# Optimization experiments

Hardware: AMD Instinct MI355X
Metric: run time of the kernel (lower is better)

## Reference

```python
import jax, jax.numpy as jnp
import numpy as np

NUM_INSTANCES = 8
NUM_HEADS = 4
EPS = 1e-12  # F.normalize eps


def _l2norm(t):
    # F.normalize(t, dim=-1): t / max(||t||_2, eps) along last axis
    n = jnp.sqrt(jnp.sum(t * t, axis=-1, keepdims=True))
    return t / jnp.maximum(n, EPS)


def setup_inputs() -> dict:
    key = jax.random.key(0)
    ks = jax.random.split(key, 10)
    B, C, H, W = 8, 256, 32, 32
    I = NUM_INSTANCES
    s = 0.05
    return {
        "x": jax.random.normal(ks[0], (B, C, H, W), dtype=jnp.float32),
        "w_inst": jax.random.normal(ks[1], (I, C), dtype=jnp.float32) * s,
        "b_inst": jnp.zeros((I,), dtype=jnp.float32),
        "w_q": jax.random.normal(ks[2], (C, C), dtype=jnp.float32) * s,
        "b_q": jnp.zeros((C,), dtype=jnp.float32),
        "w_k": jax.random.normal(ks[3], (C, C), dtype=jnp.float32) * s,
        "b_k": jnp.zeros((C,), dtype=jnp.float32),
        "w_v": jax.random.normal(ks[4], (C, C), dtype=jnp.float32) * s,
        "b_v": jnp.zeros((C,), dtype=jnp.float32),
    }


def reference(x, w_inst, b_inst, w_q, b_q, w_k, b_k, w_v, b_v):
    B, C, H, W = x.shape
    HW = H * W
    hd = C // NUM_HEADS
    scale = 1.0 / jnp.sqrt(jnp.float32(hd))

    # instance_conv (1x1) + softmax over instance axis
    inst = jnp.einsum('ic,bchw->bihw', w_inst, x) + b_inst[None, :, None, None]
    inst = jax.nn.softmax(inst, axis=1)          # [B, I, H, W]
    masks = jnp.transpose(inst, (1, 0, 2, 3))    # [I, B, H, W] for scan

    def step(acc, mask):                          # mask: [B, H, W]
        feat = (x * mask[:, None]).reshape(B, C, HW)  # masked features
        q = (jnp.einsum('oc,bcn->bon', w_q, feat) + b_q[:, None]).reshape(B, NUM_HEADS, hd, HW)
        k = (jnp.einsum('oc,bcn->bon', w_k, feat) + b_k[:, None]).reshape(B, NUM_HEADS, hd, HW)
        v = (jnp.einsum('oc,bcn->bon', w_v, feat) + b_v[:, None]).reshape(B, NUM_HEADS, hd, HW)
        q = _l2norm(q)
        k = _l2norm(k)
        scores = jnp.einsum('bhci,bhcj->bhij', q, k) * scale  # [B,h,HW,HW]
        attn = jax.nn.softmax(scores, axis=-1)
        att = jnp.einsum('bhij,bhcj->bhci', attn, v).reshape(B, C, H, W)
        return acc + att * mask[:, None], None

    out, _ = jax.lax.scan(step, jnp.zeros_like(x), masks)
    return out
```

## Files before the change

### kernel.cpp

```cpp
#include <hip/hip_runtime.h>
#include <hip/hip_fp16.h>

#define NB 8
#define NC 256
#define NHW 1024
#define NI 8
#define NH 4
#define HD 64
#define EPS 1e-12f
#define QSC  64.0f
#define QSCI 0.015625f

typedef _Float16 f16;
typedef __attribute__((ext_vector_type(8))) _Float16 half8;
typedef __attribute__((ext_vector_type(4))) float floatx4;

union H8 { half8 h8; __half2 h2[4]; uint4 u4; f16 e[8]; };
union H4 { uint2 u2; __half2 h2[2]; f16 e[4]; };
union PK { __half2 h2; unsigned u; };

__device__ __forceinline__ void gll16(const void* g, void* l) {
    __builtin_amdgcn_global_load_lds(
        (const __attribute__((address_space(1))) unsigned int*)g,
        (__attribute__((address_space(3))) unsigned int*)l, 16, 0, 0);
}

__global__ __launch_bounds__(256) void k_mask_part(
    const float* __restrict__ x, const float* __restrict__ w_inst,
    float* __restrict__ part_m, f16* __restrict__ xt)
{
    __shared__ __align__(16) f16 xls[32][264];
    int nt = blockIdx.x, b = blockIdx.y, cc = blockIdx.z;
    int tid = threadIdx.x;
    int n = nt*256 + tid;
    const float* xp = x + ((size_t)(b*NC + cc*32))*NHW + n;
    const float* wp = w_inst + cc*32;
    float acc[NI] = {};
#pragma unroll
    for (int c = 0; c < 32; ++c) {
        float xv = xp[(size_t)c*NHW];
        xls[c][tid] = (f16)xv;
#pragma unroll
        for (int i = 0; i < NI; ++i) acc[i] = fmaf(wp[i*NC + c], xv, acc[i]);
    }
#pragma unroll
    for (int i = 0; i < NI; ++i)
        part_m[((size_t)(cc*NI + i)*NB + b)*NHW + n] = acc[i];
    __syncthreads();
#pragma unroll
    for (int it = 0; it < 4; ++it) {
        int r = (tid >> 2) + it*64;
        int c8 = (tid & 3)*8;
        H8 v;
#pragma unroll
        for (int i = 0; i < 8; ++i) v.e[i] = xls[c8 + i][r];
        *(uint4*)(xt + ((size_t)(b*NHW + nt*256 + r))*NC + cc*32 + c8) = v.u4;
    }
}

__global__ __launch_bounds__(256) void k_gemm_mfma(
    const f16* __restrict__ xt,
    const float* __restrict__ wq, const float* __restrict__ wk, const float* __restrict__ wv,
    f16* __restrict__ Gqt, f16* __restrict__ Gkt, f16* __restrict__ Gv)
{
    __shared__ __align__(16) char glds[30720];
    int tid = threadIdx.x;
    int nt = blockIdx.x, ot = blockIdx.y;
    int m = blockIdx.z >> 3, b = blockIdx.z & 7;
    const float* wsel = (m == 0) ? wq : (m == 1) ? wk : wv;
    int o0 = ot*64;
    int w = tid >> 6, lane = tid & 63, quad = lane >> 4, l15 = lane & 15;
    const f16* xb = xt + (size_t)b*NHW*NC + (size_t)nt*128*NC;
    f16* wt0 = (f16*)glds;
    f16* xt0 = (f16*)(glds + 10240);
    int srow = tid >> 2, scol = (tid & 3)*8;

    floatx4 acc[2][4];
#pragma unroll
    for (int nm=0;nm<2;nm++)
#pragma unroll
        for (int om=0;om<4;om++){ acc[nm][om][0]=0.f; acc[nm][om][1]=0.f;
                                  acc[nm][om][2]=0.f; acc[nm][om][3]=0.f; }
    {
        float4 a4 = *(const float4*)(wsel + (size_t)(o0+srow)*NC + scol);
        float4 b4 = *(const float4*)(wsel + (size_t)(o0+srow)*NC + scol + 4);
        H8 hw;
        hw.h2[0] = __floats2half2_rn(a4.x, a4.y); hw.h2[1] = __floats2half2_rn(a4.z, a4.w);
        hw.h2[2] = __floats2half2_rn(b4.x, b4.y); hw.h2[3] = __floats2half2_rn(b4.z, b4.w);
        *(uint4*)&wt0[(0*64 + srow)*40 + scol] = hw.u4;
        *(uint4*)&xt0[(0*128 + srow)*40 + scol]    = *(const uint4*)(xb + (size_t)srow*NC + scol);
        *(uint4*)&xt0[(0*128 + 64+srow)*40 + scol] = *(const uint4*)(xb + (size_t)(64+srow)*NC + scol);
    }
    for (int k = 0; k < 8; ++k) {
        int p = k & 1;
        __syncthreads();
        if (k < 7) {
            int q = 1 - p, kc = (k+1)*32;
            float4 a4 = *(const float4*)(wsel + (size_t)(o0+srow)*NC + kc + scol);
            float4 b4 = *(const float4*)(wsel + (size_t)(o0+srow)*NC + kc + scol + 4);
            H8 hw;
            hw.h2[0] = __floats2half2_rn(a4.x, a4.y); hw.h2[1] = __floats2half2_rn(a4.z, a4.w);
            hw.h2[2] = __floats2half2_rn(b4.x, b4.y); hw.h2[3] = __floats2half2_rn(b4.z, b4.w);
            *(uint4*)&wt0[(q*64 + srow)*40 + scol] = hw.u4;
            *(uint4*)&xt0[(q*128 + srow)*40 + scol]    = *(const uint4*)(xb + (size_t)srow*NC + kc + scol);
            *(uint4*)&xt0[(q*128 + 64+srow)*40 + scol] = *(const uint4*)(xb + (size_t)(64+srow)*NC + kc + scol);
        }
        H8 wa[4], xa[2];
#pragma unroll
        for (int om = 0; om < 4; ++om)
            wa[om].u4 = *(const uint4*)&wt0[(p*64 + om*16 + l15)*40 + quad*8];
#pragma unroll
        for (int nm = 0; nm < 2; ++nm)
            xa[nm].u4 = *(const uint4*)&xt0[(p*128 + w*32 + nm*16 + l15)*40 + quad*8];
#pragma unroll
        for (int nm = 0; nm < 2; ++nm)
#pragma unroll
            for (int om = 0; om < 4; ++om)
                acc[nm][om] = __builtin_amdgcn_mfma_f32_16x16x32_f16(wa[om].h8, xa[nm].h8, acc[nm][om], 0, 0, 0);
    }
    __syncthreads();
    if (m < 2) {
        f16* lt = (f16*)glds;
#pragma unroll
        for (int nm = 0; nm < 2; ++nm)
#pragma unroll
            for (int om = 0; om < 4; ++om) {
                H4 pk;
#pragma unroll
                for (int r = 0; r < 4; ++r) pk.e[r] = (f16)acc[nm][om][r];
                *(uint2*)&lt[(size_t)(w*32 + nm*16 + l15)*72 + om*16 + quad*4] = pk.u2;
            }
        __syncthreads();
        f16* dst = (m == 0) ? Gqt : Gkt;
#pragma unroll
        for (int it = 0; it < 4; ++it) {
            int row = (tid >> 3) + it*32;
            int c8 = (tid & 7)*8;
            uint4 v = *(const uint4*)&lt[(size_t)row*72 + c8];
            *(uint4*)(dst + ((size_t)(b*NHW + nt*128 + row))*NC + o0 + c8) = v;
        }
    } else {
        f16* lv = (f16*)glds;
#pragma unroll
        for (int nm = 0; nm < 2; ++nm)
#pragma unroll
            for (int om = 0; om < 4; ++om)
#pragma unroll
                for (int r = 0; r < 4; ++r)
                    lv[(size_t)(om*16 + quad*4 + r)*136 + w*32 + nm*16 + l15] = (f16)acc[nm][om][r];
        __syncthreads();
#pragma unroll
        for (int it = 0; it < 4; ++it) {
            int row = (tid >> 4) + it*16;
            int n8 = (tid & 15)*8;
            uint4 v = *(const uint4*)&lv[(size_t)row*136 + n8];
            *(uint4*)(Gv + ((size_t)(b*NC + o0 + row))*NHW + nt*128 + n8) = v;
        }
    }
}

__global__ __launch_bounds__(256) void k_norm_mask(
    const float* __restrict__ part_m, const float* __restrict__ b_inst,
    const f16* __restrict__ Gqt, const f16* __restrict__ Gkt,
    const float* __restrict__ bq, const float* __restrict__ bk,
    float* __restrict__ masks, float* __restrict__ part_nq, float* __restrict__ part_nk)
{
    __shared__ float lg[NI][32];
    __shared__ __align__(16) float m_s[NI][32];
    int nc = blockIdx.x, b = blockIdx.y;
    int tid = threadIdx.x;
    int n0 = nc*32;
    {
        int nl = tid & 31, i = tid >> 5;
        float s = b_inst[i];
#pragma unroll
        for (int cc = 0; cc < 8; ++cc)
            s += part_m[((size_t)(cc*NI + i)*NB + b)*NHW + n0 + nl];
        lg[i][nl] = s;
    }
    __syncthreads();
    {
        int nl = tid & 31, i = tid >> 5;
        float mx = lg[0][nl];
#pragma unroll
        for (int k = 1; k < NI; ++k) mx = fmaxf(mx, lg[k][nl]);
        float ssum = 0.f;
#pragma unroll
        for (int k = 0; k < NI; ++k) ssum += __expf(lg[k][nl] - mx);
        float mv = __expf(lg[i][nl] - mx) / ssum;
        m_s[i][nl] = mv;
        masks[((size_t)i*NB + b)*NHW + n0 + nl] = mv;
    }
    __syncthreads();
    int c = tid;
    float bqv = bq[c], bkv = bk[c];
    const f16* gq = Gqt + ((size_t)b*NHW + n0)*NC + c;
    const f16* gk = Gkt + ((size_t)b*NHW + n0)*NC + c;
    float aq[NI] = {}, ak[NI] = {};
#pragma unroll
    for (int t4 = 0; t4 < 32; t4 += 4) {
        float g1[4], g2[4];
#pragma unroll
        for (int r = 0; r < 4; ++r) {
            g1[r] = (float)gq[(size_t)(t4 + r)*NC];
            g2[r] = (float)gk[(size_t)(t4 + r)*NC];
        }
#pragma unroll
        for (int i = 0; i < NI; ++i) {
            float4 mm4 = *(const float4*)&m_s[i][t4];
            float mm[4] = {mm4.x, mm4.y, mm4.z, mm4.w};
#pragma unroll
            for (int r = 0; r < 4; ++r) {
                float e = fmaf(mm[r], g1[r], bqv); aq[i] = fmaf(e, e, aq[i]);
                e = fmaf(mm[r], g2[r], bkv);       ak[i] = fmaf(e, e, ak[i]);
            }
        }
    }
#pragma unroll
    for (int i = 0; i < NI; ++i) {
        part_nq[((size_t)(nc*NI + i)*NB + b)*NC + c] = aq[i];
        part_nk[((size_t)(nc*NI + i)*NB + b)*NC + c] = ak[i];
    }
}

__global__ __launch_bounds__(256) void k_norm_fin(
    const float* __restrict__ part_nq, const float* __restrict__ part_nk,
    float* __restrict__ scale_q, float* __restrict__ scale_k)
{
    int b = blockIdx.x, i = blockIdx.y, c = threadIdx.x;
    float sq = 0.f, sk = 0.f;
#pragma unroll
    for (int nc = 0; nc < 32; ++nc) {
        sq += part_nq[((size_t)(nc*NI + i)*NB + b)*NC + c];
        sk += part_nk[((size_t)(nc*NI + i)*NB + b)*NC + c];
    }
    scale_q[((size_t)i*NB + b)*NC + c] = 0.125f / fmaxf(sqrtf(sq), EPS);
    scale_k[((size_t)i*NB + b)*NC + c] = 1.0f   / fmaxf(sqrtf(sk), EPS);
}

__global__ __launch_bounds__(256,2) void k_attn11(
    const f16* __restrict__ Gqt, const f16* __restrict__ Gkt, const f16* __restrict__ Gv,
    const float* __restrict__ masks,
    const float* __restrict__ bq, const float* __restrict__ bv,
    const float* __restrict__ scale_q, const float* __restrict__ scale_k,
    float* __restrict__ out)
{
    __shared__ __align__(16) char lds[38912];
    f16*   KH = (f16*)lds;
    f16*   VH = (f16*)(lds + 16384);
    float* MI = (float*)(lds + 32768);

    int tid = threadIdx.x, bid = blockIdx.x;
    int b = bid & 7, qt = (bid >> 3) & 31, h = bid >> 8;
    int qt0 = qt*32, c0 = h*HD;
    int w = tid >> 6, lane = tid & 63, quad = lane >> 4, l15 = lane & 15;
    int i0 = 2*w;

    H8 graw[2][2];
    const f16* gqp = Gqt + ((size_t)b*NHW + qt0)*NC + c0;
#pragma unroll
    for (int qi = 0; qi < 2; ++qi)
#pragma unroll
        for (int ks = 0; ks < 2; ++ks)
            graw[qi][ks].u4 = *(const uint4*)(gqp + (size_t)(qi*16 + l15)*NC + ks*32 + quad*8);
    float mqf[2][2];
#pragma unroll
    for (int ii = 0; ii < 2; ++ii)
#pragma unroll
        for (int qi = 0; qi < 2; ++qi)
            mqf[ii][qi] = masks[((size_t)(i0+ii)*NB + b)*NHW + qt0 + qi*16 + l15];
    H8 qa[2][2][2];
#pragma unroll
    for (int ks = 0; ks < 2; ++ks) {
        int cb = c0 + ks*32 + quad*8;
        float4 bq0 = *(const float4*)(bq + cb);
        float4 bq1 = *(const float4*)(bq + cb + 4);
#pragma unroll
        for (int ii = 0; ii < 2; ++ii) {
            int inst = i0 + ii;
            const float* sqg = scale_q + ((size_t)inst*NB + b)*NC;
            const float* skg = scale_k + ((size_t)inst*NB + b)*NC;
            float4 s0 = *(const float4*)(sqg + cb);
            float4 s1 = *(const float4*)(sqg + cb + 4);
            float4 t0 = *(const float4*)(skg + cb);
            float4 t1 = *(const float4*)(skg + cb + 4);
            float ss[8] = {s0.x*t0.x*QSC, s0.y*t0.y*QSC, s0.z*t0.z*QSC, s0.w*t0.w*QSC,
                           s1.x*t1.x*QSC, s1.y*t1.y*QSC, s1.z*t1.z*QSC, s1.w*t1.w*QSC};
            float bb[8] = {bq0.x*ss[0], bq0.y*ss[1], bq0.z*ss[2], bq0.w*ss[3],
                           bq1.x*ss[4], bq1.y*ss[5], bq1.z*ss[6], bq1.w*ss[7]};
            __half2 sh[4], bh[4];
#pragma unroll
            for (int t = 0; t < 4; ++t) {
                sh[t] = __floats2half2_rn(ss[2*t], ss[2*t+1]);
                bh[t] = __floats2half2_rn(bb[2*t], bb[2*t+1]);
            }
#pragma unroll
            for (int qi = 0; qi < 2; ++qi) {
                __half2 mq2 = __float2half2_rn(mqf[ii][qi]);
#pragma unroll
                for (int t = 0; t < 4; ++t)
                    qa[ii][qi][ks].h2[t] = __hfma2(mq2, __hmul2(graw[qi][ks].h2[t], sh[t]), bh[t]);
            }
        }
    }

    int kjr = tid >> 3, kdc = (tid & 7) ^ (kjr & 7);
    const f16* kgb = Gkt + (size_t)b*NHW*NC + c0 + kdc*8;
    int vcr = tid >> 3, vdc = (tid & 7) ^ (vcr & 7);
    const f16* vgb = Gv + ((size_t)(b*NC + c0 + vcr))*NHW + vdc*8;
    const float* mgb = masks + ((size_t)(tid >> 4)*NB + b)*NHW + (tid & 15)*4;

    floatx4 acc[2][4][2];
#pragma unroll
    for (int ii=0;ii<2;ii++)
#pragma unroll
        for (int cm=0;cm<4;cm++)
#pragma unroll
            for (int qi=0;qi<2;qi++) { acc[ii][cm][qi][0]=0.f; acc[ii][cm][qi][1]=0.f;
                                       acc[ii][cm][qi][2]=0.f; acc[ii][cm][qi][3]=0.f; }
    float l[2][2] = {};

    gll16(kgb + (size_t)kjr*NC,        KH + tid*8);
    gll16(kgb + (size_t)(32+kjr)*NC,   KH + 2048 + tid*8);
    gll16(vgb,                          VH + tid*8);
    gll16(vgb + (size_t)32*NHW,         VH + 2048 + tid*8);
    if (tid < 128) gll16(mgb, MI + tid*4);
    __syncthreads();

    int p = 0;
    for (int j0 = 0; j0 < NHW; j0 += 64) {
        int jn = (j0 + 64) & (NHW - 1);
        {
            f16* khn = KH + (p^1)*4096;
            f16* vhn = VH + (p^1)*4096;
            gll16(kgb + (size_t)(jn + kjr)*NC,      khn + tid*8);
            gll16(kgb + (size_t)(jn + 32 + kjr)*NC, khn + 2048 + tid*8);
            gll16(vgb + jn,                          vhn + tid*8);
            gll16(vgb + (size_t)32*NHW + jn,         vhn + 2048 + tid*8);
            if (tid < 128) gll16(mgb + jn, MI + (p^1)*512 + tid*4);
        }

        const f16* kh = KH + p*4096;
        const f16* vh = VH + p*4096;
        const float* mi = MI + p*512;

#pragma unroll
        for (int half = 0; half < 2; ++half) {
            unsigned pw[2][2][2][2];
#pragma unroll
            for (int jm2 = 0; jm2 < 2; ++jm2) {
                int jm = half*2 + jm2;
                int krow = jm*16 + l15;
                H8 ka0, ka1;
                ka0.u4 = *(const uint4*)&kh[krow*64 + ((quad       ^ (l15 & 7))*8)];
                ka1.u4 = *(const uint4*)&kh[krow*64 + (((4 + quad) ^ (l15 & 7))*8)];
#pragma unroll
                for (int ii = 0; ii < 2; ++ii) {
                    floatx4 s0 = {0.f,0.f,0.f,0.f}, s1 = {0.f,0.f,0.f,0.f};
                    s0 = __builtin_amdgcn_mfma_f32_16x16x32_f16(ka0.h8, qa[ii][0][0].h8, s0, 0, 0, 0);
                    s0 = __builtin_amdgcn_mfma_f32_16x16x32_f16(ka1.h8, qa[ii][0][1].h8, s0, 0, 0, 0);
                    s1 = __builtin_amdgcn_mfma_f32_16x16x32_f16(ka0.h8, qa[ii][1][0].h8, s1, 0, 0, 0);
                    s1 = __builtin_amdgcn_mfma_f32_16x16x32_f16(ka1.h8, qa[ii][1][1].h8, s1, 0, 0, 0);
                    float4 mj4 = *(const float4*)&mi[(i0+ii)*64 + jm*16 + quad*4];
                    float mj[4] = {mj4.x, mj4.y, mj4.z, mj4.w};
                    float p0[4], p1[4];
#pragma unroll
                    for (int r = 0; r < 4; ++r) {
                        float mq = mj[r]*QSCI;
                        float e0 = __expf(s0[r]*mq); l[ii][0] += e0; p0[r] = e0*mj[r];
                        float e1 = __expf(s1[r]*mq); l[ii][1] += e1; p1[r] = e1*mj[r];
                    }
                    PK k0, k1, k2, k3;
                    k0.h2 = __floats2half2_rn(p0[0], p0[1]); k1.h2 = __floats2half2_rn(p0[2], p0[3]);
                    k2.h2 = __floats2half2_rn(p1[0], p1[1]); k3.h2 = __floats2half2_rn(p1[2], p1[3]);
                    pw[ii][0][jm2][0] = k0.u; pw[ii][0][jm2][1] = k1.u;
                    pw[ii][1][jm2][0] = k2.u; pw[ii][1][jm2][1] = k3.u;
                }
            }
            H8 pb[2][2];
#pragma unroll
            for (int ii = 0; ii < 2; ++ii)
#pragma unroll
                for (int qi = 0; qi < 2; ++qi) {
                    unsigned a = pw[ii][qi][0][0], bx = pw[ii][qi][0][1];
                    unsigned c = pw[ii][qi][1][0], d  = pw[ii][qi][1][1];
                    asm("v_permlane32_swap_b32 %0, %1" : "+v"(a),  "+v"(c));
                    asm("v_permlane16_swap_b32 %0, %1" : "+v"(a),  "+v"(c));
                    asm("v_permlane32_swap_b32 %0, %1" : "+v"(bx), "+v"(d));
                    asm("v_permlane16_swap_b32 %0, %1" : "+v"(bx), "+v"(d));
                    H8 t; t.u4.x = a; t.u4.y = bx; t.u4.z = c; t.u4.w = d;
                    pb[ii][qi] = t;
                }
#pragma unroll
            for (int cm = 0; cm < 4; ++cm) {
                H8 va;
                va.u4 = *(const uint4*)&vh[(cm*16 + l15)*64 + (((half*4 + quad) ^ (l15 & 7))*8)];
                acc[0][cm][0] = __builtin_amdgcn_mfma_f32_16x16x32_f16(va.h8, pb[0][0].h8, acc[0][cm][0], 0, 0, 0);
                acc[0][cm][1] = __builtin_amdgcn_mfma_f32_16x16x32_f16(va.h8, pb[0][1].h8, acc[0][cm][1], 0, 0, 0);
                acc[1][cm][0] = __builtin_amdgcn_mfma_f32_16x16x32_f16(va.h8, pb[1][0].h8, acc[1][cm][0], 0, 0, 0);
                acc[1][cm][1] = __builtin_amdgcn_mfma_f32_16x16x32_f16(va.h8, pb[1][1].h8, acc[1][cm][1], 0, 0, 0);
            }
        }
        __syncthreads();
        p ^= 1;
    }

    float f[2][2];
#pragma unroll
    for (int ii = 0; ii < 2; ++ii)
#pragma unroll
        for (int qi = 0; qi < 2; ++qi) {
            float lv = l[ii][qi];
            lv += __shfl_xor(lv, 16, 64);
            lv += __shfl_xor(lv, 32, 64);
            f[ii][qi] = mqf[ii][qi] / lv;
        }
    float* bufA = (float*)lds;
    float* bufB = bufA + 2304;
    if (w < 2) {
        float* rb = w ? bufB : bufA;
#pragma unroll
        for (int cm = 0; cm < 4; ++cm)
#pragma unroll
            for (int qi = 0; qi < 2; ++qi)
#pragma unroll
                for (int r = 0; r < 4; ++r)
                    rb[(cm*16 + quad*4 + r)*36 + qi*16 + l15] =
                        f[0][qi]*acc[0][cm][qi][r] + f[1][qi]*acc[1][cm][qi][r];
    }
    __syncthreads();
    if (w >= 2) {
        float* rb = (w == 3) ? bufB : bufA;
#pragma unroll
        for (int cm = 0; cm < 4; ++cm)
#pragma unroll
            for (int qi = 0; qi < 2; ++qi)
#pragma unroll
                for (int r = 0; r < 4; ++r)
                    rb[(cm*16 + quad*4 + r)*36 + qi*16 + l15] +=
                        f[0][qi]*acc[0][cm][qi][r] + f[1][qi]*acc[1][cm][qi][r];
    }
    __syncthreads();
    int cc2 = tid >> 2, qg = (tid & 3)*8;
    float bvv = bv[c0 + cc2];
    float* op = out + ((size_t)(b*NC + c0 + cc2))*NHW + qt0;
#pragma unroll
    for (int t = 0; t < 2; ++t) {
        float4 va4 = *(const float4*)&bufA[cc2*36 + qg + t*4];
        float4 vb4 = *(const float4*)&bufB[cc2*36 + qg + t*4];
        float4 v;
        v.x = va4.x + vb4.x + bvv; v.y = va4.y + vb4.y + bvv;
        v.z = va4.z + vb4.z + bvv; v.w = va4.w + vb4.w + bvv;
        *(float4*)(op + qg + t*4) = v;
    }
}

extern "C" void kernel_launch(void* const* d_in, const int* in_sizes, int n_in,
                              void* d_out, int out_size, void* d_ws, size_t ws_size,
                              hipStream_t stream)
{
    const float* x      = (const float*)d_in[0];
    const float* w_inst = (const float*)d_in[1];
    const float* b_inst = (const float*)d_in[2];
    const float* wq = (const float*)d_in[3];
    const float* bq = (const float*)d_in[4];
    const float* wk = (const float*)d_in[5];
    const float* bk = (const float*)d_in[6];
    const float* wv = (const float*)d_in[7];
    const float* bv = (const float*)d_in[8];
    float* out = (float*)d_out;

    float* masks   = (float*)d_ws;
    float* scale_q = masks + (size_t)NI*NB*NHW;
    float* scale_k = scale_q + (size_t)NI*NB*NC;
    f16*   Gqt     = (f16*)(scale_k + (size_t)NI*NB*NC);
    f16*   Gkt     = Gqt + (size_t)NB*NHW*NC;
    f16*   Gv      = Gkt + (size_t)NB*NHW*NC;
    f16*   xt      = Gv + (size_t)NB*NC*NHW;
    float* part_m  = (float*)(xt + (size_t)NB*NHW*NC);
    float* part_nq = part_m + (size_t)8*NI*NB*NHW;
    float* part_nk = part_nq + (size_t)32*NI*NB*NC;

    k_mask_part<<<dim3(4, NB, 8), 256, 0, stream>>>(x, w_inst, part_m, xt);
    k_gemm_mfma<<<dim3(8, 4, 24), 256, 0, stream>>>(xt, wq, wk, wv, Gqt, Gkt, Gv);
    k_norm_mask<<<dim3(32, NB), 256, 0, stream>>>(part_m, b_inst, Gqt, Gkt, bq, bk,
                                                  masks, part_nq, part_nk);
    k_norm_fin<<<dim3(NB, NI), 256, 0, stream>>>(part_nq, part_nk, scale_q, scale_k);
    k_attn11<<<dim3(1024), 256, 0, stream>>>(Gqt, Gkt, Gv, masks, bq, bv,
                                             scale_q, scale_k, out);
}
```

Before: 205.9 us.

## Assign one instance per wave with 512-thread attention blocks

Result: no change. 203.0 us (median of 2 runs) (-1.4%).

```diff
diff --git a/kernel.cpp b/kernel.cpp
--- a/kernel.cpp
+++ b/kernel.cpp
@@ -238,14 +238,14 @@
     scale_k[((size_t)i*NB + b)*NC + c] = 1.0f   / fmaxf(sqrtf(sk), EPS);
 }
 
-__global__ __launch_bounds__(256,2) void k_attn11(
+__global__ __launch_bounds__(512,2) void k_attn13(
     const f16* __restrict__ Gqt, const f16* __restrict__ Gkt, const f16* __restrict__ Gv,
     const float* __restrict__ masks,
     const float* __restrict__ bq, const float* __restrict__ bv,
     const float* __restrict__ scale_q, const float* __restrict__ scale_k,
     float* __restrict__ out)
 {
-    __shared__ __align__(16) char lds[38912];
+    __shared__ __align__(16) char lds[36864];
     f16*   KH = (f16*)lds;
     f16*   VH = (f16*)(lds + 16384);
     float* MI = (float*)(lds + 32768);
@@ -254,7 +254,6 @@
     int b = bid & 7, qt = (bid >> 3) & 31, h = bid >> 8;
     int qt0 = qt*32, c0 = h*HD;
     int w = tid >> 6, lane = tid & 63, quad = lane >> 4, l15 = lane & 15;
-    int i0 = 2*w;
 
     H8 graw[2][2];
     const f16* gqp = Gqt + ((size_t)b*NHW + qt0)*NC + c0;
@@ -263,44 +262,38 @@
 #pragma unroll
         for (int ks = 0; ks < 2; ++ks)
             graw[qi][ks].u4 = *(const uint4*)(gqp + (size_t)(qi*16 + l15)*NC + ks*32 + quad*8);
-    float mqf[2][2];
-#pragma unroll
-    for (int ii = 0; ii < 2; ++ii)
-#pragma unroll
-        for (int qi = 0; qi < 2; ++qi)
-            mqf[ii][qi] = masks[((size_t)(i0+ii)*NB + b)*NHW + qt0 + qi*16 + l15];
-    H8 qa[2][2][2];
+    float mqf[2];
+#pragma unroll
+    for (int qi = 0; qi < 2; ++qi)
+        mqf[qi] = masks[((size_t)w*NB + b)*NHW + qt0 + qi*16 + l15];
+    H8 qa[2][2];
 #pragma unroll
     for (int ks = 0; ks < 2; ++ks) {
         int cb = c0 + ks*32 + quad*8;
         float4 bq0 = *(const float4*)(bq + cb);
         float4 bq1 = *(const float4*)(bq + cb + 4);
-#pragma unroll
-        for (int ii = 0; ii < 2; ++ii) {
-            int inst = i0 + ii;
-            const float* sqg = scale_q + ((size_t)inst*NB + b)*NC;
-            const float* skg = scale_k + ((size_t)inst*NB + b)*NC;
-            float4 s0 = *(const float4*)(sqg + cb);
-            float4 s1 = *(const float4*)(sqg + cb + 4);
-            float4 t0 = *(const float4*)(skg + cb);
-            float4 t1 = *(const float4*)(skg + cb + 4);
-            float ss[8] = {s0.x*t0.x*QSC, s0.y*t0.y*QSC, s0.z*t0.z*QSC, s0.w*t0.w*QSC,
-                           s1.x*t1.x*QSC, s1.y*t1.y*QSC, s1.z*t1.z*QSC, s1.w*t1.w*QSC};
-            float bb[8] = {bq0.x*ss[0], bq0.y*ss[1], bq0.z*ss[2], bq0.w*ss[3],
-                           bq1.x*ss[4], bq1.y*ss[5], bq1.z*ss[6], bq1.w*ss[7]};
-            __half2 sh[4], bh[4];
-#pragma unroll
-            for (int t = 0; t < 4; ++t) {
-                sh[t] = __floats2half2_rn(ss[2*t], ss[2*t+1]);
-                bh[t] = __floats2half2_rn(bb[2*t], bb[2*t+1]);
-            }
-#pragma unroll
-            for (int qi = 0; qi < 2; ++qi) {
-                __half2 mq2 = __float2half2_rn(mqf[ii][qi]);
-#pragma unroll
-                for (int t = 0; t < 4; ++t)
-                    qa[ii][qi][ks].h2[t] = __hfma2(mq2, __hmul2(graw[qi][ks].h2[t], sh[t]), bh[t]);
-            }
+        const float* sqg = scale_q + ((size_t)w*NB + b)*NC;
+        const float* skg = scale_k + ((size_t)w*NB + b)*NC;
+        float4 s0 = *(const float4*)(sqg + cb);
+        float4 s1 = *(const float4*)(sqg + cb + 4);
+        float4 t0 = *(const float4*)(skg + cb);
+        float4 t1 = *(const float4*)(skg + cb + 4);
+        float ss[8] = {s0.x*t0.x*QSC, s0.y*t0.y*QSC, s0.z*t0.z*QSC, s0.w*t0.w*QSC,
+                       s1.x*t1.x*QSC, s1.y*t1.y*QSC, s1.z*t1.z*QSC, s1.w*t1.w*QSC};
+        float bb[8] = {bq0.x*ss[0], bq0.y*ss[1], bq0.z*ss[2], bq0.w*ss[3],
+                       bq1.x*ss[4], bq1.y*ss[5], bq1.z*ss[6], bq1.w*ss[7]};
+        __half2 sh[4], bh[4];
+#pragma unroll
+        for (int t = 0; t < 4; ++t) {
+            sh[t] = __floats2half2_rn(ss[2*t], ss[2*t+1]);
+            bh[t] = __floats2half2_rn(bb[2*t], bb[2*t+1]);
+        }
+#pragma unroll
+        for (int qi = 0; qi < 2; ++qi) {
+            __half2 mq2 = __float2half2_rn(mqf[qi]);
+#pragma unroll
+            for (int t = 0; t < 4; ++t)
+                qa[qi][ks].h2[t] = __hfma2(mq2, __hmul2(graw[qi][ks].h2[t], sh[t]), bh[t]);
         }
     }
 
@@ -310,35 +303,25 @@
     const f16* vgb = Gv + ((size_t)(b*NC + c0 + vcr))*NHW + vdc*8;
     const float* mgb = masks + ((size_t)(tid >> 4)*NB + b)*NHW + (tid & 15)*4;
 
-    floatx4 acc[2][4][2];
-#pragma unroll
-    for (int ii=0;ii<2;ii++)
-#pragma unroll
-        for (int cm=0;cm<4;cm++)
-#pragma unroll
-            for (int qi=0;qi<2;qi++) { acc[ii][cm][qi][0]=0.f; acc[ii][cm][qi][1]=0.f;
-                                       acc[ii][cm][qi][2]=0.f; acc[ii][cm][qi][3]=0.f; }
-    float l[2][2] = {};
-
-    gll16(kgb + (size_t)kjr*NC,        KH + tid*8);
-    gll16(kgb + (size_t)(32+kjr)*NC,   KH + 2048 + tid*8);
-    gll16(vgb,                          VH + tid*8);
-    gll16(vgb + (size_t)32*NHW,         VH + 2048 + tid*8);
+    floatx4 acc[4][2];
+#pragma unroll
+    for (int cm=0;cm<4;cm++)
+#pragma unroll
+        for (int qi=0;qi<2;qi++) { acc[cm][qi][0]=0.f; acc[cm][qi][1]=0.f;
+                                   acc[cm][qi][2]=0.f; acc[cm][qi][3]=0.f; }
+    float l[2] = {};
+
+    gll16(kgb + (size_t)kjr*NC, KH + tid*8);
+    gll16(vgb,                  VH + tid*8);
     if (tid < 128) gll16(mgb, MI + tid*4);
     __syncthreads();
 
     int p = 0;
     for (int j0 = 0; j0 < NHW; j0 += 64) {
         int jn = (j0 + 64) & (NHW - 1);
-        {
-            f16* khn = KH + (p^1)*4096;
-            f16* vhn = VH + (p^1)*4096;
-            gll16(kgb + (size_t)(jn + kjr)*NC,      khn + tid*8);
-            gll16(kgb + (size_t)(jn + 32 + kjr)*NC, khn + 2048 + tid*8);
-            gll16(vgb + jn,                          vhn + tid*8);
-            gll16(vgb + (size_t)32*NHW + jn,         vhn + 2048 + tid*8);
-            if (tid < 128) gll16(mgb + jn, MI + (p^1)*512 + tid*4);
-        }
+        gll16(kgb + (size_t)(jn + kjr)*NC, KH + (p^1)*4096 + tid*8);
+        gll16(vgb + jn,                    VH + (p^1)*4096 + tid*8);
+        if (tid < 128) gll16(mgb + jn, MI + (p^1)*512 + tid*4);
 
         const f16* kh = KH + p*4096;
         const f16* vh = VH + p*4096;
@@ -346,7 +329,7 @@
 
 #pragma unroll
         for (int half = 0; half < 2; ++half) {
-            unsigned pw[2][2][2][2];
+            unsigned pw[2][2][2];
 #pragma unroll
             for (int jm2 = 0; jm2 < 2; ++jm2) {
                 int jm = half*2 + jm2;
@@ -354,105 +337,92 @@
                 H8 ka0, ka1;
                 ka0.u4 = *(const uint4*)&kh[krow*64 + ((quad       ^ (l15 & 7))*8)];
                 ka1.u4 = *(const uint4*)&kh[krow*64 + (((4 + quad) ^ (l15 & 7))*8)];
-#pragma unroll
-                for (int ii = 0; ii < 2; ++ii) {
-                    floatx4 s0 = {0.f,0.f,0.f,0.f}, s1 = {0.f,0.f,0.f,0.f};
-                    s0 = __builtin_amdgcn_mfma_f32_16x16x32_f16(ka0.h8, qa[ii][0][0].h8, s0, 0, 0, 0);
-                    s0 = __builtin_amdgcn_mfma_f32_16x16x32_f16(ka1.h8, qa[ii][0][1].h8, s0, 0, 0, 0);
-                    s1 = __builtin_amdgcn_mfma_f32_16x16x32_f16(ka0.h8, qa[ii][1][0].h8, s1, 0, 0, 0);
-                    s1 = __builtin_amdgcn_mfma_f32_16x16x32_f16(ka1.h8, qa[ii][1][1].h8, s1, 0, 0, 0);
-                    float4 mj4 = *(const float4*)&mi[(i0+ii)*64 + jm*16 + quad*4];
-                    float mj[4] = {mj4.x, mj4.y, mj4.z, mj4.w};
-                    float p0[4], p1[4];
-#pragma unroll
-                    for (int r = 0; r < 4; ++r) {
-                        float mq = mj[r]*QSCI;
-                        float e0 = __expf(s0[r]*mq); l[ii][0] += e0; p0[r] = e0*mj[r];
-                        float e1 = __expf(s1[r]*mq); l[ii][1] += e1; p1[r] = e1*mj[r];
-                    }
-                    PK k0, k1, k2, k3;
-                    k0.h2 = __floats2half2_rn(p0[0], p0[1]); k1.h2 = __floats2half2_rn(p0[2], p0[3]);
-                    k2.h2 = __floats2half2_rn(p1[0], p1[1]); k3.h2 = __floats2half2_rn(p1[2], p1[3]);
-                    pw[ii][0][jm2][0] = k0.u; pw[ii][0][jm2][1] = k1.u;
-                    pw[ii][1][jm2][0] = k2.u; pw[ii][1][jm2][1] = k3.u;
+                floatx4 s0 = {0.f,0.f,0.f,0.f}, s1 = {0.f,0.f,0.f,0.f};
+                s0 = __builtin_amdgcn_mfma_f32_16x16x32_f16(ka0.h8, qa[0][0].h8, s0, 0, 0, 0);
+                s0 = __builtin_amdgcn_mfma_f32_16x16x32_f16(ka1.h8, qa[0][1].h8, s0, 0, 0, 0);
+                s1 = __builtin_amdgcn_mfma_f32_16x16x32_f16(ka0.h8, qa[1][0].h8, s1, 0, 0, 0);
+                s1 = __builtin_amdgcn_mfma_f32_16x16x32_f16(ka1.h8, qa[1][1].h8, s1, 0, 0, 0);
+                float4 mj4 = *(const float4*)&mi[w*64 + jm*16 + quad*4];
+                float mj[4] = {mj4.x, mj4.y, mj4.z, mj4.w};
+                float p0[4], p1[4];
+#pragma unroll
+                for (int r = 0; r < 4; ++r) {
+                    float mq = mj[r]*QSCI;
+                    float e0 = __expf(s0[r]*mq); l[0] += e0; p0[r] = e0*mj[r];
+                    float e1 = __expf(s1[r]*mq); l[1] += e1; p1[r] = e1*mj[r];
                 }
+                PK k0, k1, k2, k3;
+                k0.h2 = __floats2half2_rn(p0[0], p0[1]); k1.h2 = __floats2half2_rn(p0[2], p0[3]);
+                k2.h2 = __floats2half2_rn(p1[0], p1[1]); k3.h2 = __floats2half2_rn(p1[2], p1[3]);
+                pw[0][jm2][0] = k0.u; pw[0][jm2][1] = k1.u;
+                pw[1][jm2][0] = k2.u; pw[1][jm2][1] = k3.u;
             }
-            H8 pb[2][2];
-#pragma unroll
-            for (int ii = 0; ii < 2; ++ii)
-#pragma unroll
-                for (int qi = 0; qi < 2; ++qi) {
-                    unsigned a = pw[ii][qi][0][0], bx = pw[ii][qi][0][1];
-                    unsigned c = pw[ii][qi][1][0], d  = pw[ii][qi][1][1];
-                    asm("v_permlane32_swap_b32 %0, %1" : "+v"(a),  "+v"(c));
-                    asm("v_permlane16_swap_b32 %0, %1" : "+v"(a),  "+v"(c));
-                    asm("v_permlane32_swap_b32 %0, %1" : "+v"(bx), "+v"(d));
-                    asm("v_permlane16_swap_b32 %0, %1" : "+v"(bx), "+v"(d));
-                    H8 t; t.u4.x = a; t.u4.y = bx; t.u4.z = c; t.u4.w = d;
-                    pb[ii][qi] = t;
-                }
+            H8 pb[2];
+#pragma unroll
+            for (int qi = 0; qi < 2; ++qi) {
+                unsigned a = pw[qi][0][0], bx = pw[qi][0][1];
+                unsigned c = pw[qi][1][0], d  = pw[qi][1][1];
+                asm("v_permlane32_swap_b32 %0, %1" : "+v"(a),  "+v"(c));
+                asm("v_permlane16_swap_b32 %0, %1" : "+v"(a),  "+v"(c));
+                asm("v_permlane32_swap_b32 %0, %1" : "+v"(bx), "+v"(d));
+                asm("v_permlane16_swap_b32 %0, %1" : "+v"(bx), "+v"(d));
+                H8 t; t.u4.x = a; t.u4.y = bx; t.u4.z = c; t.u4.w = d;
+                pb[qi] = t;
+            }
 #pragma unroll
             for (int cm = 0; cm < 4; ++cm) {
                 H8 va;
                 va.u4 = *(const uint4*)&vh[(cm*16 + l15)*64 + (((half*4 + quad) ^ (l15 & 7))*8)];
-                acc[0][cm][0] = __builtin_amdgcn_mfma_f32_16x16x32_f16(va.h8, pb[0][0].h8, acc[0][cm][0], 0, 0, 0);
-                acc[0][cm][1] = __builtin_amdgcn_mfma_f32_16x16x32_f16(va.h8, pb[0][1].h8, acc[0][cm][1], 0, 0, 0);
-                acc[1][cm][0] = __builtin_amdgcn_mfma_f32_16x16x32_f16(va.h8, pb[1][0].h8, acc[1][cm][0], 0, 0, 0);
-                acc[1][cm][1] = __builtin_amdgcn_mfma_f32_16x16x32_f16(va.h8, pb[1][1].h8, acc[1][cm][1], 0, 0, 0);
+                acc[cm][0] = __builtin_amdgcn_mfma_f32_16x16x32_f16(va.h8, pb[0].h8, acc[cm][0], 0, 0, 0);
+                acc[cm][1] = __builtin_amdgcn_mfma_f32_16x16x32_f16(va.h8, pb[1].h8, acc[cm][1], 0, 0, 0);
             }
         }
         __syncthreads();
         p ^= 1;
     }
 
-    float f[2][2];
-#pragma unroll
-    for (int ii = 0; ii < 2; ++ii)
-#pragma unroll
-        for (int qi = 0; qi < 2; ++qi) {
-            float lv = l[ii][qi];
-            lv += __shfl_xor(lv, 16, 64);
-            lv += __shfl_xor(lv, 32, 64);
-            f[ii][qi] = mqf[ii][qi] / lv;
-        }
-    float* bufA = (float*)lds;
-    float* bufB = bufA + 2304;
-    if (w < 2) {
-        float* rb = w ? bufB : bufA;
+    float f[2];
+#pragma unroll
+    for (int qi = 0; qi < 2; ++qi) {
+        float lv = l[qi];
+        lv += __shfl_xor(lv, 16, 64);
+        lv += __shfl_xor(lv, 32, 64);
+        f[qi] = mqf[qi] / lv;
+    }
+    float* rb = (float*)lds + (size_t)(w & 3)*2304;
+    if (w < 4) {
 #pragma unroll
         for (int cm = 0; cm < 4; ++cm)
 #pragma unroll
             for (int qi = 0; qi < 2; ++qi)
 #pragma unroll
                 for (int r = 0; r < 4; ++r)
-                    rb[(cm*16 + quad*4 + r)*36 + qi*16 + l15] =
-                        f[0][qi]*acc[0][cm][qi][r] + f[1][qi]*acc[1][cm][qi][r];
-    }
-    __syncthreads();
-    if (w >= 2) {
-        float* rb = (w == 3) ? bufB : bufA;
+                    rb[(cm*16 + quad*4 + r)*36 + qi*16 + l15] = f[qi]*acc[cm][qi][r];
+    }
+    __syncthreads();
+    if (w >= 4) {
 #pragma unroll
         for (int cm = 0; cm < 4; ++cm)
 #pragma unroll
             for (int qi = 0; qi < 2; ++qi)
 #pragma unroll
                 for (int r = 0; r < 4; ++r)
-                    rb[(cm*16 + quad*4 + r)*36 + qi*16 + l15] +=
-                        f[0][qi]*acc[0][cm][qi][r] + f[1][qi]*acc[1][cm][qi][r];
-    }
-    __syncthreads();
-    int cc2 = tid >> 2, qg = (tid & 3)*8;
+                    rb[(cm*16 + quad*4 + r)*36 + qi*16 + l15] += f[qi]*acc[cm][qi][r];
+    }
+    __syncthreads();
+    int cc2 = tid >> 3, qg = (tid & 7)*4;
     float bvv = bv[c0 + cc2];
-    float* op = out + ((size_t)(b*NC + c0 + cc2))*NHW + qt0;
-#pragma unroll
-    for (int t = 0; t < 2; ++t) {
-        float4 va4 = *(const float4*)&bufA[cc2*36 + qg + t*4];
-        float4 vb4 = *(const float4*)&bufB[cc2*36 + qg + t*4];
-        float4 v;
-        v.x = va4.x + vb4.x + bvv; v.y = va4.y + vb4.y + bvv;
-        v.z = va4.z + vb4.z + bvv; v.w = va4.w + vb4.w + bvv;
-        *(float4*)(op + qg + t*4) = v;
-    }
+    const float* b0 = (const float*)lds;
+    float4 v0 = *(const float4*)&b0[cc2*36 + qg];
+    float4 v1 = *(const float4*)&b0[2304 + cc2*36 + qg];
+    float4 v2 = *(const float4*)&b0[4608 + cc2*36 + qg];
+    float4 v3 = *(const float4*)&b0[6912 + cc2*36 + qg];
+    float4 v;
+    v.x = v0.x + v1.x + v2.x + v3.x + bvv;
+    v.y = v0.y + v1.y + v2.y + v3.y + bvv;
+    v.z = v0.z + v1.z + v2.z + v3.z + bvv;
+    v.w = v0.w + v1.w + v2.w + v3.w + bvv;
+    *(float4*)(out + ((size_t)(b*NC + c0 + cc2))*NHW + qt0 + qg) = v;
 }
 
 extern "C" void kernel_launch(void* const* d_in, const int* in_sizes, int n_in,
@@ -486,6 +456,6 @@
     k_norm_mask<<<dim3(32, NB), 256, 0, stream>>>(part_m, b_inst, Gqt, Gkt, bq, bk,
                                                   masks, part_nq, part_nk);
     k_norm_fin<<<dim3(NB, NI), 256, 0, stream>>>(part_nq, part_nk, scale_q, scale_k);
-    k_attn11<<<dim3(1024), 256, 0, stream>>>(Gqt, Gkt, Gv, masks, bq, bv,
+    k_attn13<<<dim3(1024), 512, 0, stream>>>(Gqt, Gkt, Gv, masks, bq, bv,
                                              scale_q, scale_k, out);
 }
```
